# Kernel optimization log

Measured on AMD Instinct MI355X. Metric: run time of the kernel, lower is better.

Reference implementation:

```python
import jax, jax.numpy as jnp
import numpy as np

NUM_EXPERTS = 8
D_MODEL = 1024
D_HIDDEN = 4096
TOP_K = 2
BATCH, SEQ = 2, 4096
T = BATCH * SEQ


def setup_inputs() -> dict:
    key = jax.random.key(0)
    k_x, k_p, k_i, k_wu, k_wd = jax.random.split(key, 5)
    x = jax.random.normal(k_x, (BATCH, SEQ, D_MODEL), dtype=jnp.float32)
    p = jax.random.uniform(k_p, (T, TOP_K), dtype=jnp.float32)
    expert_p = p / jnp.sum(p, axis=-1, keepdims=True)  # normalized gates over top-k
    expert_idxs = jax.random.randint(k_i, (T, TOP_K), 0, NUM_EXPERTS, dtype=jnp.int64)
    # ParallelExperts weight banks (stored as [E, in, out] for x @ W convention)
    w_up = jax.random.normal(k_wu, (NUM_EXPERTS, D_MODEL, D_HIDDEN), dtype=jnp.float32) * (D_MODEL ** -0.5)
    w_down = jax.random.normal(k_wd, (NUM_EXPERTS, D_HIDDEN, D_MODEL), dtype=jnp.float32) * (D_HIDDEN ** -0.5)
    return {"x": x, "expert_p": expert_p, "expert_idxs": expert_idxs,
            "w_up": w_up, "w_down": w_down}


def reference(x, expert_p, expert_idxs, w_up, w_down):
    """MoE MLP: for each token t and each of its top-k experts e=idx[t,k]:
       y[t] += p[t,k] * (gelu(x[t] @ Wup[e]) @ Wdown[e]).
       Expressed as a loop over the small fixed expert set with per-expert
       gate masses (mathematically identical to sort+grouped-GEMM dispatch)."""
    x_shape = x.shape
    xf = x.reshape(-1, x_shape[-1])  # [T, d]
    num_experts = w_up.shape[0]
    y = jnp.zeros_like(xf)
    for e in range(num_experts):
        # total gate mass routed from each token to expert e (0 if not routed)
        gate_e = jnp.sum(expert_p * (expert_idxs == e), axis=-1)  # [T]
        h = jax.nn.gelu(xf @ w_up[e], approximate=False)          # [T, hidden]
        y = y + gate_e[:, None] * (h @ w_down[e])                 # [T, d]
    return y.reshape(x_shape)
```

## Files before the change

### kernel.cpp

```cpp
#include <hip/hip_runtime.h>
#include <hip/hip_bf16.h>
#include <stdint.h>

#define NE 8
#define DM 1024
#define DH 4096
#define T_TOK 8192
#define NA 16384
#define BM 256
#define BN 256
#define BK 64
#define MAX_TILES 16

typedef __attribute__((ext_vector_type(8))) short short8;
typedef __attribute__((ext_vector_type(4))) float f32x4;

typedef const __attribute__((address_space(1))) void cas1void;
typedef __attribute__((address_space(3))) void as3void;
#define GL2L(gp, lp) __builtin_amdgcn_global_load_lds((cas1void*)(uintptr_t)(gp), (as3void*)(uintptr_t)(lp), 16, 0, 0)

__device__ __forceinline__ unsigned short f2bf(float f) {
  union { float f; unsigned u; } v; v.f = f;
  unsigned r = (v.u + 0x7FFFu + ((v.u >> 16) & 1u)) >> 16;
  return (unsigned short)r;
}
__device__ __forceinline__ float geluf(float x) {
  float u = 0.7978845608028654f * x * (1.0f + 0.044715f * x * x);
  return x / (1.0f + __expf(-2.0f * u));
}

__global__ void k_route(const int* __restrict__ idx, const float* __restrict__ p,
                        int* __restrict__ offs, int* __restrict__ btok,
                        float* __restrict__ gate) {
  __shared__ int cnt[NE], cur[NE], off_s[NE];
  int tid = threadIdx.x;
  if (tid < NE) { cnt[tid] = 0; cur[tid] = 0; }
  __syncthreads();
  int e_loc[NA / 1024];
#pragma unroll
  for (int i = 0; i < NA / 1024; ++i) {
    int a = i * 1024 + tid;
    e_loc[i] = idx[a];
    atomicAdd(&cnt[e_loc[i]], 1);
  }
  __syncthreads();
  if (tid == 0) {
    int s = 0;
    for (int e = 0; e < NE; ++e) { off_s[e] = s; offs[e] = s; s += cnt[e]; }
    offs[NE] = s;
  }
  __syncthreads();
#pragma unroll
  for (int i = 0; i < NA / 1024; ++i) {
    int a = i * 1024 + tid;
    int e = e_loc[i];
    int pos = off_s[e] + atomicAdd(&cur[e], 1);
    btok[pos] = a >> 1;
    gate[pos] = p[a];
  }
}

__global__ void k_cvt_x(const float* __restrict__ x, unsigned short* __restrict__ xb) {
  int i = (blockIdx.x * 256 + threadIdx.x) * 8;
  float4 v0 = *(const float4*)(x + i);
  float4 v1 = *(const float4*)(x + i + 4);
  ushort4 o0, o1;
  o0.x = f2bf(v0.x); o0.y = f2bf(v0.y); o0.z = f2bf(v0.z); o0.w = f2bf(v0.w);
  o1.x = f2bf(v1.x); o1.y = f2bf(v1.y); o1.z = f2bf(v1.z); o1.w = f2bf(v1.w);
  *(ushort4*)(xb + i) = o0;
  *(ushort4*)(xb + i + 4) = o1;
}

__global__ void k_transpose2(const float* __restrict__ wup, const float* __restrict__ wdn,
                             unsigned short* __restrict__ wupT, unsigned short* __restrict__ wdnT) {
  __shared__ float tile[64][65];
  int z = blockIdx.z;
  const float* src; unsigned short* dst; int C, R, c0, r0;
  if (z < NE) {
    src = wup + (size_t)z * DM * DH; dst = wupT + (size_t)z * DM * DH;
    R = DM; C = DH; c0 = blockIdx.x * 64; r0 = blockIdx.y * 64;
  } else {
    src = wdn + (size_t)(z - NE) * DM * DH; dst = wdnT + (size_t)(z - NE) * DM * DH;
    R = DH; C = DM; c0 = (blockIdx.x & 15) * 64; r0 = (blockIdx.y * 4 + (blockIdx.x >> 4)) * 64;
  }
  int tid = threadIdx.x;
  int tr = tid >> 4;
  int tc = (tid & 15) * 4;
#pragma unroll
  for (int rr = 0; rr < 64; rr += 16) {
    float4 v = *(const float4*)(src + (size_t)(r0 + tr + rr) * C + c0 + tc);
    tile[tr + rr][tc + 0] = v.x; tile[tr + rr][tc + 1] = v.y;
    tile[tr + rr][tc + 2] = v.z; tile[tr + rr][tc + 3] = v.w;
  }
  __syncthreads();
#pragma unroll
  for (int cc = 0; cc < 64; cc += 16) {
    int oc = tr + cc;
    ushort4 o;
    o.x = f2bf(tile[tc + 0][oc]); o.y = f2bf(tile[tc + 1][oc]);
    o.z = f2bf(tile[tc + 2][oc]); o.w = f2bf(tile[tc + 3][oc]);
    *(ushort4*)(dst + (size_t)(c0 + oc) * R + r0 + tc) = o;
  }
}

#define STG2(P, S, D, RB, KT)                                                   \
  {                                                                             \
    GL2L(P[RB] + (KT) * BK, &S[D][((RB) * 64 + wrow) * BK]);                    \
    GL2L(P[(RB) + 1] + (KT) * BK, &S[D][(((RB) + 1) * 64 + wrow) * BK]);        \
  }

#define RDA(D, QM)                                                              \
  _Pragma("unroll") for (int kk = 0; kk < 2; ++kk) {                            \
    int so_ = sw0 ^ (kk << 5);                                                  \
    _Pragma("unroll") for (int i = 0; i < 4; ++i)                               \
      av[i][kk] = *(const short8*)&sA[D][((QM) * 128 + wm * 64 + lr) * BK + i * 16 * BK + so_]; \
  }
#define RDB(D, QN, BV)                                                          \
  _Pragma("unroll") for (int kk = 0; kk < 2; ++kk) {                            \
    int so_ = sw0 ^ (kk << 5);                                                  \
    _Pragma("unroll") for (int j = 0; j < 2; ++j)                               \
      BV[j][kk] = *(const short8*)&sB[D][((QN) * 128 + wn * 32 + lr) * BK + j * 16 * BK + so_]; \
  }
#define MM(QM, QN, BV)                                                          \
  _Pragma("unroll") for (int kk = 0; kk < 2; ++kk)                              \
    _Pragma("unroll") for (int i = 0; i < 4; ++i)                               \
      _Pragma("unroll") for (int j = 0; j < 2; ++j)                             \
        acc[QM][QN][i][j] = __builtin_amdgcn_mfma_f32_16x16x32_bf16(            \
            av[i][kk], BV[j][kk], acc[QM][QN][i][j], 0, 0, 0);

#define VM4 asm volatile("s_waitcnt vmcnt(4)" ::: "memory")
#define VM0 asm volatile("s_waitcnt vmcnt(0)" ::: "memory")
#define LG0 asm volatile("s_waitcnt lgkmcnt(0)" ::: "memory")

template <int NT>
__device__ __forceinline__ void gemm_pipe(const unsigned short* const (&pA)[4],
                                          const unsigned short* const (&pB)[4],
                                          short (&sA)[2][BM * BK], short (&sB)[2][BN * BK],
                                          int wrow, int wm, int wn, int lr, int sw0,
                                          f32x4 (&acc)[2][2][4][2]) {
  short8 av[4][2], b0[2][2], b1[2][2];
  STG2(pA, sA, 0, 0, 0); STG2(pA, sA, 0, 2, 0);
  STG2(pB, sB, 0, 0, 0); STG2(pB, sB, 0, 2, 0);
  STG2(pA, sA, 1, 0, 1); STG2(pB, sB, 1, 0, 1);
  VM4;
  __builtin_amdgcn_s_barrier();
#pragma unroll 1
  for (int t0 = 0; t0 < NT; t0 += 2) {
    const int t1 = t0 + 1;
    const bool s05 = (t0 + 2 < NT);
    const bool s67 = (t1 + 2 < NT);
    RDA(0, 0); RDB(0, 0, b0);
    STG2(pA, sA, 1, 2, t1); STG2(pB, sB, 1, 2, t1);
    LG0;
    __builtin_amdgcn_s_barrier();
    if (s05) { STG2(pA, sA, 0, 0, t0 + 2); STG2(pB, sB, 0, 0, t0 + 2); }
    MM(0, 0, b0);
    RDB(0, 1, b1);
    MM(0, 1, b1);
    RDA(0, 1);
    MM(1, 0, b0);
    MM(1, 1, b1);
    if (s05) { VM4; } else { VM0; }
    __builtin_amdgcn_s_barrier();
    RDA(1, 0); RDB(1, 0, b0);
    if (s05) { STG2(pA, sA, 0, 2, t0 + 2); STG2(pB, sB, 0, 2, t0 + 2); }
    LG0;
    __builtin_amdgcn_s_barrier();
    if (s67) { STG2(pA, sA, 1, 0, t1 + 2); STG2(pB, sB, 1, 0, t1 + 2); }
    MM(0, 0, b0);
    RDB(1, 1, b1);
    MM(0, 1, b1);
    RDA(1, 1);
    MM(1, 0, b0);
    MM(1, 1, b1);
    VM4;
    __builtin_amdgcn_s_barrier();
  }
}

__global__ __launch_bounds__(512, 2) void k_up(
    const unsigned short* __restrict__ xb, const unsigned short* __restrict__ wupT,
    const int* __restrict__ offs, const int* __restrict__ btok,
    unsigned short* __restrict__ h) {
  int e = blockIdx.x & 7;
  int r = blockIdx.x >> 3;
  int ny = r & 15, tile = r >> 4;
  int beg = offs[e], cnt = offs[e + 1] - beg;
  int m0 = tile * BM;
  if (m0 >= cnt) return;
  int n0 = ny * BN;
  __align__(16) __shared__ short sA[2][BM * BK];
  __align__(16) __shared__ short sB[2][BN * BK];
  int tid = threadIdx.x;
  int w = tid >> 6, lane = tid & 63;
  int wm = w >> 2, wn = w & 3;
  int wrow = w << 3;
  int swcol = (((tid & 7) ^ ((tid >> 3) & 7)) << 3);
  const unsigned short* pA[4];
  const unsigned short* pB[4];
#pragma unroll
  for (int rr = 0; rr < 4; ++rr) {
    int arow = rr * 64 + (tid >> 3);
    int tok = btok[beg + min(m0 + arow, cnt - 1)];
    pA[rr] = xb + (size_t)tok * DM + swcol;
    pB[rr] = wupT + ((size_t)e * DH + n0 + arow) * DM + swcol;
  }
  int lr = lane & 15, lg = lane >> 4;
  int sw0 = (lg << 3) ^ ((lr & 7) << 3);
  f32x4 acc[2][2][4][2];
#pragma unroll
  for (int qm = 0; qm < 2; ++qm)
#pragma unroll
    for (int qn = 0; qn < 2; ++qn)
#pragma unroll
      for (int i = 0; i < 4; ++i)
#pragma unroll
        for (int j = 0; j < 2; ++j) acc[qm][qn][i][j] = (f32x4){0.f, 0.f, 0.f, 0.f};

  gemm_pipe<DM / BK>(pA, pB, sA, sB, wrow, wm, wn, lr, sw0, acc);

#pragma unroll
  for (int qm = 0; qm < 2; ++qm)
#pragma unroll
    for (int qn = 0; qn < 2; ++qn)
#pragma unroll
      for (int i = 0; i < 4; ++i)
#pragma unroll
        for (int q = 0; q < 4; ++q) {
          int grow = qm * 128 + wm * 64 + i * 16 + lg * 4 + q;
          if (m0 + grow < cnt) {
            size_t orow = (size_t)(beg + m0 + grow) * DH + n0;
#pragma unroll
            for (int j = 0; j < 2; ++j) {
              int col = qn * 128 + wn * 32 + j * 16 + lr;
              h[orow + col] = f2bf(geluf(acc[qm][qn][i][j][q]));
            }
          }
        }
}

__global__ __launch_bounds__(512, 2) void k_down(
    const unsigned short* __restrict__ h, const unsigned short* __restrict__ wdnT,
    const int* __restrict__ offs, const int* __restrict__ btok,
    const float* __restrict__ gate, float* __restrict__ y) {
  int e = blockIdx.x & 7;
  int r = blockIdx.x >> 3;
  int ny = r & 3;
  int td = r >> 2;
  int tile = td >> 1, ks = td & 1;
  int beg = offs[e], cnt = offs[e + 1] - beg;
  int m0 = tile * BM;
  if (m0 >= cnt) return;
  int n0 = ny * BN;
  __align__(16) __shared__ short sA[2][BM * BK];
  __align__(16) __shared__ short sB[2][BN * BK];
  __shared__ int s_tok[BM];
  __shared__ float s_g[BM];
  int tid = threadIdx.x;
  if (tid < BM) {
    int rr = min(m0 + tid, cnt - 1);
    s_tok[tid] = btok[beg + rr];
    s_g[tid] = gate[beg + rr];
  }
  __syncthreads();
  int w = tid >> 6, lane = tid & 63;
  int wm = w >> 2, wn = w & 3;
  int wrow = w << 3;
  int swcol = (((tid & 7) ^ ((tid >> 3) & 7)) << 3);
  const int kbase = ks * (DH / 2);
  const unsigned short* pA[4];
  const unsigned short* pB[4];
#pragma unroll
  for (int rr = 0; rr < 4; ++rr) {
    int arow = rr * 64 + (tid >> 3);
    int slot = beg + min(m0 + arow, cnt - 1);
    pA[rr] = h + (size_t)slot * DH + kbase + swcol;
    pB[rr] = wdnT + ((size_t)e * DM + n0 + arow) * DH + kbase + swcol;
  }
  int lr = lane & 15, lg = lane >> 4;
  int sw0 = (lg << 3) ^ ((lr & 7) << 3);
  f32x4 acc[2][2][4][2];
#pragma unroll
  for (int qm = 0; qm < 2; ++qm)
#pragma unroll
    for (int qn = 0; qn < 2; ++qn)
#pragma unroll
      for (int i = 0; i < 4; ++i)
#pragma unroll
        for (int j = 0; j < 2; ++j) acc[qm][qn][i][j] = (f32x4){0.f, 0.f, 0.f, 0.f};

  gemm_pipe<DH / (2 * BK)>(pA, pB, sA, sB, wrow, wm, wn, lr, sw0, acc);

#pragma unroll
  for (int qm = 0; qm < 2; ++qm)
#pragma unroll
    for (int qn = 0; qn < 2; ++qn)
#pragma unroll
      for (int i = 0; i < 4; ++i)
#pragma unroll
        for (int q = 0; q < 4; ++q) {
          int grow = qm * 128 + wm * 64 + i * 16 + lg * 4 + q;
          if (m0 + grow < cnt) {
            float g2 = s_g[grow];
            int tk = s_tok[grow];
#pragma unroll
            for (int j = 0; j < 2; ++j) {
              int col = n0 + qn * 128 + wn * 32 + j * 16 + lr;
              atomicAdd(&y[(size_t)tk * DM + col], acc[qm][qn][i][j][q] * g2);
            }
          }
        }
}

extern "C" void kernel_launch(void* const* d_in, const int* in_sizes, int n_in,
                              void* d_out, int out_size, void* d_ws, size_t ws_size,
                              hipStream_t stream) {
  (void)in_sizes; (void)n_in; (void)ws_size;
  const float* x   = (const float*)d_in[0];
  const float* p   = (const float*)d_in[1];
  const int*   idx = (const int*)d_in[2];
  const float* wup = (const float*)d_in[3];
  const float* wdn = (const float*)d_in[4];
  float* y = (float*)d_out;
  char* ws = (char*)d_ws;
  int* offs   = (int*)(ws + 128);
  int* btok   = (int*)(ws + 256);
  float* gate = (float*)(ws + 256 + 65536);
  unsigned short* xb   = (unsigned short*)(ws + 131328);
  unsigned short* wupT = (unsigned short*)(ws + 131328 + 16777216);
  unsigned short* wdnT = wupT + (size_t)NE * DH * DM;
  unsigned short* h    = wdnT + (size_t)NE * DM * DH;

  hipMemsetAsync(d_out, 0, (size_t)out_size * sizeof(float), stream);
  k_route<<<1, 1024, 0, stream>>>(idx, p, offs, btok, gate);
  k_cvt_x<<<(T_TOK * DM) / (256 * 8), 256, 0, stream>>>(x, xb);
  k_transpose2<<<dim3(64, 16, 2 * NE), 256, 0, stream>>>(wup, wdn, wupT, wdnT);
  k_up<<<MAX_TILES * 16 * NE, 512, 0, stream>>>(xb, wupT, offs, btok, h);
  k_down<<<(MAX_TILES * 2) * 4 * NE, 512, 0, stream>>>(h, wdnT, offs, btok, gate, y);
}
```

Before: 535.7 us.

## Replace 256x256 pipelined expert GEMM with simpler 128x128 tiles and 4-way split-K

```diff
diff --git a/kernel.cpp b/kernel.cpp
--- a/kernel.cpp
+++ b/kernel.cpp
@@ -7,10 +7,10 @@
 #define DH 4096
 #define T_TOK 8192
 #define NA 16384
-#define BM 256
-#define BN 256
+#define BM 128
+#define BN 128
 #define BK 64
-#define MAX_TILES 16
+#define MT 20
 
 typedef __attribute__((ext_vector_type(8))) short short8;
 typedef __attribute__((ext_vector_type(4))) float f32x4;
@@ -103,157 +103,111 @@
   }
 }
 
-#define STG2(P, S, D, RB, KT)                                                   \
-  {                                                                             \
-    GL2L(P[RB] + (KT) * BK, &S[D][((RB) * 64 + wrow) * BK]);                    \
-    GL2L(P[(RB) + 1] + (KT) * BK, &S[D][(((RB) + 1) * 64 + wrow) * BK]);        \
-  }
-
-#define RDA(D, QM)                                                              \
-  _Pragma("unroll") for (int kk = 0; kk < 2; ++kk) {                            \
-    int so_ = sw0 ^ (kk << 5);                                                  \
-    _Pragma("unroll") for (int i = 0; i < 4; ++i)                               \
-      av[i][kk] = *(const short8*)&sA[D][((QM) * 128 + wm * 64 + lr) * BK + i * 16 * BK + so_]; \
-  }
-#define RDB(D, QN, BV)                                                          \
-  _Pragma("unroll") for (int kk = 0; kk < 2; ++kk) {                            \
-    int so_ = sw0 ^ (kk << 5);                                                  \
-    _Pragma("unroll") for (int j = 0; j < 2; ++j)                               \
-      BV[j][kk] = *(const short8*)&sB[D][((QN) * 128 + wn * 32 + lr) * BK + j * 16 * BK + so_]; \
-  }
-#define MM(QM, QN, BV)                                                          \
-  _Pragma("unroll") for (int kk = 0; kk < 2; ++kk)                              \
-    _Pragma("unroll") for (int i = 0; i < 4; ++i)                               \
-      _Pragma("unroll") for (int j = 0; j < 2; ++j)                             \
-        acc[QM][QN][i][j] = __builtin_amdgcn_mfma_f32_16x16x32_bf16(            \
-            av[i][kk], BV[j][kk], acc[QM][QN][i][j], 0, 0, 0);
-
-#define VM4 asm volatile("s_waitcnt vmcnt(4)" ::: "memory")
-#define VM0 asm volatile("s_waitcnt vmcnt(0)" ::: "memory")
-#define LG0 asm volatile("s_waitcnt lgkmcnt(0)" ::: "memory")
-
-template <int NT>
-__device__ __forceinline__ void gemm_pipe(const unsigned short* const (&pA)[4],
-                                          const unsigned short* const (&pB)[4],
-                                          short (&sA)[2][BM * BK], short (&sB)[2][BN * BK],
-                                          int wrow, int wm, int wn, int lr, int sw0,
-                                          f32x4 (&acc)[2][2][4][2]) {
-  short8 av[4][2], b0[2][2], b1[2][2];
-  STG2(pA, sA, 0, 0, 0); STG2(pA, sA, 0, 2, 0);
-  STG2(pB, sB, 0, 0, 0); STG2(pB, sB, 0, 2, 0);
-  STG2(pA, sA, 1, 0, 1); STG2(pB, sB, 1, 0, 1);
-  VM4;
-  __builtin_amdgcn_s_barrier();
+template <int NKT>
+__device__ __forceinline__ void gemm128(const unsigned short* const (&pA)[4],
+                                        const unsigned short* const (&pB)[4],
+                                        short* sA, short* sB, int w, int lane,
+                                        f32x4 (&acc)[4][4]) {
+  int wm = w & 1, wn = w >> 1;
+  int lr = lane & 15, lg = lane >> 4;
+  int wbase = w << 3;
+  int arow = (wm * 64 + lr) * 64;
+  int brow = (wn * 64 + lr) * 64;
+  int swz = ((lr & 7) << 3);
 #pragma unroll 1
-  for (int t0 = 0; t0 < NT; t0 += 2) {
-    const int t1 = t0 + 1;
-    const bool s05 = (t0 + 2 < NT);
-    const bool s67 = (t1 + 2 < NT);
-    RDA(0, 0); RDB(0, 0, b0);
-    STG2(pA, sA, 1, 2, t1); STG2(pB, sB, 1, 2, t1);
-    LG0;
-    __builtin_amdgcn_s_barrier();
-    if (s05) { STG2(pA, sA, 0, 0, t0 + 2); STG2(pB, sB, 0, 0, t0 + 2); }
-    MM(0, 0, b0);
-    RDB(0, 1, b1);
-    MM(0, 1, b1);
-    RDA(0, 1);
-    MM(1, 0, b0);
-    MM(1, 1, b1);
-    if (s05) { VM4; } else { VM0; }
-    __builtin_amdgcn_s_barrier();
-    RDA(1, 0); RDB(1, 0, b0);
-    if (s05) { STG2(pA, sA, 0, 2, t0 + 2); STG2(pB, sB, 0, 2, t0 + 2); }
-    LG0;
-    __builtin_amdgcn_s_barrier();
-    if (s67) { STG2(pA, sA, 1, 0, t1 + 2); STG2(pB, sB, 1, 0, t1 + 2); }
-    MM(0, 0, b0);
-    RDB(1, 1, b1);
-    MM(0, 1, b1);
-    RDA(1, 1);
-    MM(1, 0, b0);
-    MM(1, 1, b1);
-    VM4;
-    __builtin_amdgcn_s_barrier();
-  }
-}
-
-__global__ __launch_bounds__(512, 2) void k_up(
+  for (int kt = 0; kt < NKT; ++kt) {
+#pragma unroll
+    for (int r = 0; r < 4; ++r) {
+      GL2L(pA[r] + kt * BK, sA + (r * 32 + wbase) * 64);
+      GL2L(pB[r] + kt * BK, sB + (r * 32 + wbase) * 64);
+    }
+    __syncthreads();
+#pragma unroll
+    for (int kk = 0; kk < 2; ++kk) {
+      int co = ((kk << 5) | (lg << 3)) ^ swz;
+      short8 av[4], bv[4];
+#pragma unroll
+      for (int i = 0; i < 4; ++i) av[i] = *(const short8*)&sA[arow + i * 16 * 64 + co];
+#pragma unroll
+      for (int j = 0; j < 4; ++j) bv[j] = *(const short8*)&sB[brow + j * 16 * 64 + co];
+#pragma unroll
+      for (int i = 0; i < 4; ++i)
+#pragma unroll
+        for (int j = 0; j < 4; ++j)
+          acc[i][j] = __builtin_amdgcn_mfma_f32_16x16x32_bf16(av[i], bv[j], acc[i][j], 0, 0, 0);
+    }
+    __syncthreads();
+  }
+}
+
+__global__ __launch_bounds__(256, 3) void k_up(
     const unsigned short* __restrict__ xb, const unsigned short* __restrict__ wupT,
     const int* __restrict__ offs, const int* __restrict__ btok,
     unsigned short* __restrict__ h) {
   int e = blockIdx.x & 7;
   int r = blockIdx.x >> 3;
-  int ny = r & 15, tile = r >> 4;
+  int tile = r % MT, ny = r / MT;
   int beg = offs[e], cnt = offs[e + 1] - beg;
   int m0 = tile * BM;
   if (m0 >= cnt) return;
   int n0 = ny * BN;
-  __align__(16) __shared__ short sA[2][BM * BK];
-  __align__(16) __shared__ short sB[2][BN * BK];
+  __align__(16) __shared__ short sA[BM * BK];
+  __align__(16) __shared__ short sB[BN * BK];
   int tid = threadIdx.x;
   int w = tid >> 6, lane = tid & 63;
-  int wm = w >> 2, wn = w & 3;
-  int wrow = w << 3;
-  int swcol = (((tid & 7) ^ ((tid >> 3) & 7)) << 3);
+  int grp = tid >> 3, gran = tid & 7;
+  int swcol = ((gran ^ (grp & 7)) << 3);
   const unsigned short* pA[4];
   const unsigned short* pB[4];
 #pragma unroll
   for (int rr = 0; rr < 4; ++rr) {
-    int arow = rr * 64 + (tid >> 3);
-    int tok = btok[beg + min(m0 + arow, cnt - 1)];
+    int row = rr * 32 + grp;
+    int tok = btok[beg + min(m0 + row, cnt - 1)];
     pA[rr] = xb + (size_t)tok * DM + swcol;
-    pB[rr] = wupT + ((size_t)e * DH + n0 + arow) * DM + swcol;
-  }
+    pB[rr] = wupT + ((size_t)e * DH + n0 + row) * DM + swcol;
+  }
+  f32x4 acc[4][4];
+#pragma unroll
+  for (int i = 0; i < 4; ++i)
+#pragma unroll
+    for (int j = 0; j < 4; ++j) acc[i][j] = (f32x4){0.f, 0.f, 0.f, 0.f};
+
+  gemm128<DM / BK>(pA, pB, sA, sB, w, lane, acc);
+
+  int wm = w & 1, wn = w >> 1;
   int lr = lane & 15, lg = lane >> 4;
-  int sw0 = (lg << 3) ^ ((lr & 7) << 3);
-  f32x4 acc[2][2][4][2];
-#pragma unroll
-  for (int qm = 0; qm < 2; ++qm)
-#pragma unroll
-    for (int qn = 0; qn < 2; ++qn)
-#pragma unroll
-      for (int i = 0; i < 4; ++i)
-#pragma unroll
-        for (int j = 0; j < 2; ++j) acc[qm][qn][i][j] = (f32x4){0.f, 0.f, 0.f, 0.f};
-
-  gemm_pipe<DM / BK>(pA, pB, sA, sB, wrow, wm, wn, lr, sw0, acc);
-
-#pragma unroll
-  for (int qm = 0; qm < 2; ++qm)
-#pragma unroll
-    for (int qn = 0; qn < 2; ++qn)
-#pragma unroll
-      for (int i = 0; i < 4; ++i)
-#pragma unroll
-        for (int q = 0; q < 4; ++q) {
-          int grow = qm * 128 + wm * 64 + i * 16 + lg * 4 + q;
-          if (m0 + grow < cnt) {
-            size_t orow = (size_t)(beg + m0 + grow) * DH + n0;
-#pragma unroll
-            for (int j = 0; j < 2; ++j) {
-              int col = qn * 128 + wn * 32 + j * 16 + lr;
-              h[orow + col] = f2bf(geluf(acc[qm][qn][i][j][q]));
-            }
-          }
+#pragma unroll
+  for (int i = 0; i < 4; ++i)
+#pragma unroll
+    for (int q = 0; q < 4; ++q) {
+      int grow = wm * 64 + i * 16 + lg * 4 + q;
+      if (m0 + grow < cnt) {
+        size_t orow = (size_t)(beg + m0 + grow) * DH + n0;
+#pragma unroll
+        for (int j = 0; j < 4; ++j) {
+          int col = wn * 64 + j * 16 + lr;
+          h[orow + col] = f2bf(geluf(acc[i][j][q]));
         }
-}
-
-__global__ __launch_bounds__(512, 2) void k_down(
+      }
+    }
+}
+
+__global__ __launch_bounds__(256, 3) void k_down(
     const unsigned short* __restrict__ h, const unsigned short* __restrict__ wdnT,
     const int* __restrict__ offs, const int* __restrict__ btok,
     const float* __restrict__ gate, float* __restrict__ y) {
   int e = blockIdx.x & 7;
   int r = blockIdx.x >> 3;
-  int ny = r & 3;
-  int td = r >> 2;
-  int tile = td >> 1, ks = td & 1;
+  int tile = r % MT;
+  int q2 = r / MT;
+  int ny = q2 & 7, ks = q2 >> 3;
   int beg = offs[e], cnt = offs[e + 1] - beg;
   int m0 = tile * BM;
   if (m0 >= cnt) return;
   int n0 = ny * BN;
-  __align__(16) __shared__ short sA[2][BM * BK];
-  __align__(16) __shared__ short sB[2][BN * BK];
+  int kbase = ks * (DH / 4);
+  __align__(16) __shared__ short sA[BM * BK];
+  __align__(16) __shared__ short sB[BN * BK];
   __shared__ int s_tok[BM];
   __shared__ float s_g[BM];
   int tid = threadIdx.x;
@@ -262,54 +216,43 @@
     s_tok[tid] = btok[beg + rr];
     s_g[tid] = gate[beg + rr];
   }
-  __syncthreads();
   int w = tid >> 6, lane = tid & 63;
-  int wm = w >> 2, wn = w & 3;
-  int wrow = w << 3;
-  int swcol = (((tid & 7) ^ ((tid >> 3) & 7)) << 3);
-  const int kbase = ks * (DH / 2);
+  int grp = tid >> 3, gran = tid & 7;
+  int swcol = ((gran ^ (grp & 7)) << 3);
   const unsigned short* pA[4];
   const unsigned short* pB[4];
 #pragma unroll
   for (int rr = 0; rr < 4; ++rr) {
-    int arow = rr * 64 + (tid >> 3);
-    int slot = beg + min(m0 + arow, cnt - 1);
+    int row = rr * 32 + grp;
+    int slot = beg + min(m0 + row, cnt - 1);
     pA[rr] = h + (size_t)slot * DH + kbase + swcol;
-    pB[rr] = wdnT + ((size_t)e * DM + n0 + arow) * DH + kbase + swcol;
-  }
+    pB[rr] = wdnT + ((size_t)e * DM + n0 + row) * DH + kbase + swcol;
+  }
+  f32x4 acc[4][4];
+#pragma unroll
+  for (int i = 0; i < 4; ++i)
+#pragma unroll
+    for (int j = 0; j < 4; ++j) acc[i][j] = (f32x4){0.f, 0.f, 0.f, 0.f};
+
+  gemm128<(DH / 4) / BK>(pA, pB, sA, sB, w, lane, acc);
+
+  int wm = w & 1, wn = w >> 1;
   int lr = lane & 15, lg = lane >> 4;
-  int sw0 = (lg << 3) ^ ((lr & 7) << 3);
-  f32x4 acc[2][2][4][2];
-#pragma unroll
-  for (int qm = 0; qm < 2; ++qm)
-#pragma unroll
-    for (int qn = 0; qn < 2; ++qn)
-#pragma unroll
-      for (int i = 0; i < 4; ++i)
-#pragma unroll
-        for (int j = 0; j < 2; ++j) acc[qm][qn][i][j] = (f32x4){0.f, 0.f, 0.f, 0.f};
-
-  gemm_pipe<DH / (2 * BK)>(pA, pB, sA, sB, wrow, wm, wn, lr, sw0, acc);
-
-#pragma unroll
-  for (int qm = 0; qm < 2; ++qm)
-#pragma unroll
-    for (int qn = 0; qn < 2; ++qn)
-#pragma unroll
-      for (int i = 0; i < 4; ++i)
-#pragma unroll
-        for (int q = 0; q < 4; ++q) {
-          int grow = qm * 128 + wm * 64 + i * 16 + lg * 4 + q;
-          if (m0 + grow < cnt) {
-            float g2 = s_g[grow];
-            int tk = s_tok[grow];
-#pragma unroll
-            for (int j = 0; j < 2; ++j) {
-              int col = n0 + qn * 128 + wn * 32 + j * 16 + lr;
-              atomicAdd(&y[(size_t)tk * DM + col], acc[qm][qn][i][j][q] * g2);
-            }
-          }
+#pragma unroll
+  for (int i = 0; i < 4; ++i)
+#pragma unroll
+    for (int q = 0; q < 4; ++q) {
+      int grow = wm * 64 + i * 16 + lg * 4 + q;
+      if (m0 + grow < cnt) {
+        float g2 = s_g[grow];
+        int tk = s_tok[grow];
+#pragma unroll
+        for (int j = 0; j < 4; ++j) {
+          int col = n0 + wn * 64 + j * 16 + lr;
+          atomicAdd(&y[(size_t)tk * DM + col], acc[i][j][q] * g2);
         }
+      }
+    }
 }
 
 extern "C" void kernel_launch(void* const* d_in, const int* in_sizes, int n_in,
@@ -335,6 +278,6 @@
   k_route<<<1, 1024, 0, stream>>>(idx, p, offs, btok, gate);
   k_cvt_x<<<(T_TOK * DM) / (256 * 8), 256, 0, stream>>>(x, xb);
   k_transpose2<<<dim3(64, 16, 2 * NE), 256, 0, stream>>>(wup, wdn, wupT, wdnT);
-  k_up<<<MAX_TILES * 16 * NE, 512, 0, stream>>>(xb, wupT, offs, btok, h);
-  k_down<<<(MAX_TILES * 2) * 4 * NE, 512, 0, stream>>>(h, wdnT, offs, btok, gate, y);
-}
+  k_up<<<NE * MT * 32, 256, 0, stream>>>(xb, wupT, offs, btok, h);
+  k_down<<<NE * MT * 32, 256, 0, stream>>>(h, wdnT, offs, btok, gate, y);
+}
```

After: 534.9 us. No clear change (-0.2%).
